# Kernel optimization log

Measured on AMD Instinct MI355X. Metric: run time of the kernel, lower is better.

The kernel has to match this reference:

```python
import jax, jax.numpy as jnp
import numpy as np

B, S, D, H = 2, 2048, 1024, 16
EPS = 1e-7  # keras backend epsilon

def setup_inputs() -> dict:
    key = jax.random.key(0)
    ks = jax.random.split(key, 5)
    x = jax.random.normal(ks[0], (B, S, D), dtype=jnp.float32)
    # mem_mask convention: attend where mem_mask == 0 (causal here)
    i = jnp.arange(S)
    causal = (i[None, :] > i[:, None]).astype(jnp.float32)  # 1 = masked
    mem_mask = jnp.broadcast_to(causal[None, None], (B, 1, S, S))
    Wqkv = jax.random.normal(ks[1], (D, 3 * D), dtype=jnp.float32) * (D ** -0.5)
    W_out = jax.random.normal(ks[2], (D, D), dtype=jnp.float32) * (D ** -0.5)
    b_out = jnp.zeros((D,), dtype=jnp.float32)
    scale = jnp.ones((D,), dtype=jnp.float32)
    gate = jax.random.normal(ks[3], (D,), dtype=jnp.float32) * 0.02
    return {"x": x, "mem_mask": mem_mask, "Wqkv": Wqkv, "W_out": W_out,
            "b_out": b_out, "scale": scale, "gate": gate}

def reference(x, mem_mask, Wqkv, W_out, b_out, scale, gate):
    b, s, d = x.shape
    dh = d // H
    h = jnp.einsum('bsd,de->bse', x, Wqkv)
    q, k, v = jnp.split(h, 3, axis=-1)
    def split_heads(t):
        return t.reshape(b, s, H, dh).transpose(0, 2, 1, 3)  # [B,H,S,dh]
    q, k, v = split_heads(q), split_heads(k), split_heads(v)
    q = q * (dh ** -0.5)
    logits = jnp.einsum('bhqd,bhkd->bhqk', q, k)
    logits = logits * (mem_mask == 0.0).astype(logits.dtype)
    weights = jax.nn.relu(logits)
    o = jnp.einsum('bhqk,bhkd->bhqd', weights, v)
    o = o.transpose(0, 2, 1, 3).reshape(b, s, d)  # combine heads
    # Gated RMSNorm
    ms = jnp.mean(o * o, axis=-1, keepdims=True)
    o = scale * o * jax.lax.rsqrt(ms + EPS) * jax.nn.sigmoid(gate * o)
    return jnp.einsum('bsd,de->bse', o, W_out) + b_out
```

## Files before the change

kernel.cpp:

```cpp
#include <hip/hip_runtime.h>
#include <hip/hip_bf16.h>

typedef unsigned short u16;
typedef __attribute__((ext_vector_type(8))) short bf16x8;
typedef __attribute__((ext_vector_type(4))) short short4v;
typedef __attribute__((ext_vector_type(4))) float floatx4;
typedef __attribute__((ext_vector_type(2))) unsigned uint2v;

__device__ __forceinline__ float bf2f(u16 u) {
    unsigned v = ((unsigned)u) << 16;
    return __builtin_bit_cast(float, v);
}
__device__ __forceinline__ u16 f2bf(float f) {
    unsigned u = __builtin_bit_cast(unsigned, f);
    u += 0x7fffu + ((u >> 16) & 1u);
    return (u16)(u >> 16);
}

#define GLDS16(g, l)                                                             \
    __builtin_amdgcn_global_load_lds(                                            \
        (const __attribute__((address_space(1))) void*)(g),                      \
        (__attribute__((address_space(3))) void*)(l), 16, 0, 0)

__global__ __launch_bounds__(256) void prep(const float* __restrict__ x, u16* __restrict__ xb,
                                            const float* __restrict__ Wqkv, u16* __restrict__ WqkvT,
                                            const float* __restrict__ Wout, u16* __restrict__ WoutT) {
    __shared__ u16 t[32][33];
    int blk = blockIdx.x;
    if (blk < 4096) {
        const int i = blk * 256 + threadIdx.x;
        const floatx4 v = ((const floatx4*)x)[i];
        short4v o;
#pragma unroll
        for (int j = 0; j < 4; ++j) o[j] = (short)f2bf(v[j]);
        ((short4v*)xb)[i] = o;
        return;
    }
    const float* in; u16* out; int R, C, bx, by;
    if (blk < 4096 + 3072) { blk -= 4096; in = Wqkv; out = WqkvT; R = 1024; C = 3072; bx = blk % 96; by = blk / 96; }
    else                   { blk -= 7168; in = Wout; out = WoutT; R = 1024; C = 1024; bx = blk & 31; by = blk >> 5; }
    const int c0 = bx * 32, r0 = by * 32;
    const int xx = threadIdx.x & 31, yy = threadIdx.x >> 5;
#pragma unroll
    for (int i = 0; i < 32; i += 8) t[yy + i][xx] = f2bf(in[(size_t)(r0 + yy + i) * C + c0 + xx]);
    __syncthreads();
#pragma unroll
    for (int i = 0; i < 32; i += 8) out[(size_t)(c0 + yy + i) * R + r0 + xx] = t[xx][yy + i];
}

template <int TM, bool BIAS, typename OUT, bool VT>
__global__ __launch_bounds__(256) void gemm_bt(const u16* __restrict__ A, const u16* __restrict__ Bt,
                                               OUT* __restrict__ C, const float* __restrict__ bias,
                                               u16* __restrict__ vtp, int M, int N, int K) {
    constexpr int MI = TM / 32;
    __shared__ u16 sA[TM * 32];
    __shared__ u16 sB[128 * 32];
    const int tid = threadIdx.x;
    const int lane = tid & 63, wave = tid >> 6;
    const int l15 = lane & 15, quad = lane >> 4;
    const int row0 = blockIdx.y * TM, col0 = blockIdx.x * 128;
    const int wm = (wave & 1) * (TM / 2), wn = (wave >> 1) * 64;
    const int c_ = (tid & 3) << 3;
    floatx4 acc[MI][4] = {};
    for (int k0 = 0; k0 < K; k0 += 32) {
#pragma unroll
        for (int it = 0; it < 2; ++it) {
            const int idx = it * 256 + tid;
            const int r = idx >> 2;
            GLDS16(Bt + (size_t)(col0 + r) * K + k0 + c_, sB + idx * 8);
        }
#pragma unroll
        for (int it = 0; it < TM / 64; ++it) {
            const int idx = it * 256 + tid;
            const int r = idx >> 2;
            GLDS16(A + (size_t)(row0 + r) * K + k0 + c_, sA + idx * 8);
        }
        __syncthreads();
        bf16x8 af[MI], bfr[4];
#pragma unroll
        for (int i = 0; i < MI; ++i) af[i] = *(const bf16x8*)(sA + (wm + i * 16 + l15) * 32 + quad * 8);
#pragma unroll
        for (int j = 0; j < 4; ++j) bfr[j] = *(const bf16x8*)(sB + (wn + j * 16 + l15) * 32 + quad * 8);
#pragma unroll
        for (int i = 0; i < MI; ++i)
#pragma unroll
            for (int j = 0; j < 4; ++j)
                acc[i][j] = __builtin_amdgcn_mfma_f32_16x16x32_bf16(af[i], bfr[j], acc[i][j], 0, 0, 0);
        __syncthreads();
    }
#pragma unroll
    for (int i = 0; i < MI; ++i) {
#pragma unroll
        for (int j = 0; j < 4; ++j) {
            const int col = col0 + wn + j * 16 + l15;
            const int row = row0 + wm + i * 16 + quad * 4;
            const float b = BIAS ? bias[col] : 0.f;
            short4v pk;
#pragma unroll
            for (int r = 0; r < 4; ++r) {
                const float v = acc[i][j][r] + b;
                if constexpr (sizeof(OUT) == 2)
                    C[(size_t)(row + r) * N + col] = (OUT)f2bf(v);
                else
                    C[(size_t)(row + r) * N + col] = (OUT)v;
                if constexpr (VT) pk[r] = (short)f2bf(v * 0.125f);
            }
            if constexpr (VT) {
                if (col0 >= 2048) {
                    const int bb = row >> 11, s = row & 2047;
                    const int hd = (col - 2048) >> 6, dh = col & 63;
                    *(short4v*)(vtp + ((size_t)(bb * 16 + hd) * 64 + dh) * 2048 + s) = pk;
                }
            }
        }
    }
}

__device__ __forceinline__ void pack_store(floatx4 s, u16* dst, bool diag, int kgb, int qg) {
    float v0 = fmaxf(s[0], 0.f), v1 = fmaxf(s[1], 0.f);
    float v2 = fmaxf(s[2], 0.f), v3 = fmaxf(s[3], 0.f);
    if (diag) {
        if (kgb + 0 > qg) v0 = 0.f;
        if (kgb + 1 > qg) v1 = 0.f;
        if (kgb + 2 > qg) v2 = 0.f;
        if (kgb + 3 > qg) v3 = 0.f;
    }
    uint2v p;
    p.x = ((__builtin_bit_cast(unsigned, v0) + 0x8000u) >> 16) |
          ((__builtin_bit_cast(unsigned, v1) + 0x8000u) & 0xffff0000u);
    p.y = ((__builtin_bit_cast(unsigned, v2) + 0x8000u) >> 16) |
          ((__builtin_bit_cast(unsigned, v3) + 0x8000u) & 0xffff0000u);
    *(uint2v*)dst = p;
}

__global__ __launch_bounds__(256) void relu_attn(const u16* __restrict__ h, const u16* __restrict__ vt,
                                                 float* __restrict__ o) {
    __shared__ u16 sK[2][64 * 64];
    __shared__ u16 sV[2][64 * 64];
    __shared__ u16 sP[128 * 72];
    const int bid = blockIdx.x;
    const int pr = bid >> 5;
    const int bh = bid & 31;
    const int b = bh >> 4, hd = bh & 15;
    const int qtl = pr, qth = 31 - pr;
    const int tid = threadIdx.x, lane = tid & 63, wave = tid >> 6;
    const int l15 = lane & 15, quad = lane >> 4;
    const int swz = l15 & 7;

    bf16x8 qfl[2], qfh[2];
    {
        const u16* ql = h + (size_t)(b * 2048 + qtl * 64 + wave * 16 + l15) * 3072 + hd * 64;
        const u16* qh = h + (size_t)(b * 2048 + qth * 64 + wave * 16 + l15) * 3072 + hd * 64;
#pragma unroll
        for (int ks = 0; ks < 2; ++ks) {
            qfl[ks] = *(const bf16x8*)(ql + ks * 32 + quad * 8);
            qfh[ks] = *(const bf16x8*)(qh + ks * 32 + quad * 8);
        }
    }

    floatx4 accl[4] = {}, acch[4] = {};
    const u16* kbase = h + (size_t)(b * 2048) * 3072 + 1024 + hd * 64;
    const u16* vbase = vt + (size_t)bh * 64 * 2048;
    const int qg = wave * 16 + l15;

    auto stage = [&](int kc, int bufi) {
#pragma unroll
        for (int it = 0; it < 2; ++it) {
            const int idx = it * 256 + tid;
            const int r = idx >> 3;
            const int cg = (idx & 7) ^ (r & 7);
            GLDS16(kbase + (size_t)(kc * 64 + r) * 3072 + cg * 8, &sK[bufi][idx * 8]);
            GLDS16(vbase + (size_t)r * 2048 + kc * 64 + cg * 8, &sV[bufi][idx * 8]);
        }
    };

    stage(0, 0);
    __syncthreads();

    for (int kc = 0; kc <= qth; ++kc) {
        const int cur = kc & 1;
        if (kc < qth) stage(kc + 1, cur ^ 1);
        const u16* sKb = sK[cur];
        const u16* sVb = sV[cur];
        const bool lact = (kc <= qtl);
        const floatx4 z = {0.f, 0.f, 0.f, 0.f};
        const int c0 = kc * 64;
#pragma unroll
        for (int mt = 0; mt < 4; ++mt) {
            const int R = mt * 16 + l15;
            const int cq = quad ^ swz;
            const bf16x8 kf0 = *(const bf16x8*)(sKb + R * 64 + cq * 8);
            const bf16x8 kf1 = *(const bf16x8*)(sKb + R * 64 + (cq ^ 4) * 8);
            const int kgb = mt * 16 + quad * 4;
            floatx4 s = __builtin_amdgcn_mfma_f32_16x16x32_bf16(kf0, qfh[0], z, 0, 0, 0);
            s = __builtin_amdgcn_mfma_f32_16x16x32_bf16(kf1, qfh[1], s, 0, 0, 0);
            pack_store(s, sP + (size_t)(64 + qg) * 72 + kgb, kc == qth, kgb, qg);
            if (lact) {
                floatx4 t = __builtin_amdgcn_mfma_f32_16x16x32_bf16(kf0, qfl[0], z, 0, 0, 0);
                t = __builtin_amdgcn_mfma_f32_16x16x32_bf16(kf1, qfl[1], t, 0, 0, 0);
                pack_store(t, sP + (size_t)qg * 72 + kgb, kc == qtl, kgb, qg);
            }
        }
#pragma unroll
        for (int kb = 0; kb < 2; ++kb) {
            const bf16x8 pfh = *(const bf16x8*)(sP + (size_t)(64 + wave * 16 + l15) * 72 + kb * 32 + quad * 8);
#pragma unroll
            for (int nt = 0; nt < 4; ++nt) {
                const int cv = ((kb << 2) | quad) ^ swz;
                const bf16x8 vf = *(const bf16x8*)(sVb + (nt * 16 + l15) * 64 + cv * 8);
                acch[nt] = __builtin_amdgcn_mfma_f32_16x16x32_bf16(pfh, vf, acch[nt], 0, 0, 0);
                if (lact) {
                    const bf16x8 pfl = *(const bf16x8*)(sP + (size_t)(wave * 16 + l15) * 72 + kb * 32 + quad * 8);
                    accl[nt] = __builtin_amdgcn_mfma_f32_16x16x32_bf16(pfl, vf, accl[nt], 0, 0, 0);
                }
            }
        }
        __syncthreads();
    }
#pragma unroll
    for (int nt = 0; nt < 4; ++nt) {
        const int col = hd * 64 + nt * 16 + l15;
        const int rl = qtl * 64 + wave * 16 + quad * 4;
        const int rh = qth * 64 + wave * 16 + quad * 4;
#pragma unroll
        for (int r = 0; r < 4; ++r) {
            o[(size_t)(b * 2048 + rl + r) * 1024 + col] = accl[nt][r];
            o[(size_t)(b * 2048 + rh + r) * 1024 + col] = acch[nt][r];
        }
    }
}

__global__ __launch_bounds__(256) void rms_gate(const float* __restrict__ o, const float* __restrict__ scale,
                                                const float* __restrict__ gate, u16* __restrict__ out) {
    const int row = blockIdx.x;
    const int tid = threadIdx.x;
    const floatx4* op = (const floatx4*)(o + (size_t)row * 1024);
    floatx4 v = op[tid];
    float ss = v[0] * v[0] + v[1] * v[1] + v[2] * v[2] + v[3] * v[3];
#pragma unroll
    for (int m = 32; m >= 1; m >>= 1) ss += __shfl_xor(ss, m, 64);
    __shared__ float red[4];
    if ((tid & 63) == 0) red[tid >> 6] = ss;
    __syncthreads();
    const float ms = (red[0] + red[1] + red[2] + red[3]) * (1.0f / 1024.0f);
    const float inv = rsqrtf(ms + 1e-7f);
    const int c = tid * 4;
#pragma unroll
    for (int j = 0; j < 4; ++j) {
        const float s = scale[c + j];
        const float g = gate[c + j];
        const float x = v[j];
        const float sig = 1.0f / (1.0f + __expf(-g * x));
        out[(size_t)row * 1024 + c + j] = f2bf(s * x * inv * sig);
    }
}

extern "C" void kernel_launch(void* const* d_in, const int* in_sizes, int n_in,
                              void* d_out, int out_size, void* d_ws, size_t ws_size,
                              hipStream_t stream) {
    const float* x     = (const float*)d_in[0];
    const float* Wqkv  = (const float*)d_in[2];
    const float* Wout  = (const float*)d_in[3];
    const float* bout  = (const float*)d_in[4];
    const float* scale = (const float*)d_in[5];
    const float* gate  = (const float*)d_in[6];
    float* out = (float*)d_out;

    char* p = (char*)d_ws;
    u16* xb    = (u16*)p; p += (size_t)4096 * 1024 * 2;
    u16* h     = (u16*)p; p += (size_t)4096 * 3072 * 2;
    u16* vt    = (u16*)p; p += (size_t)32 * 64 * 2048 * 2;
    u16* WqkvT = (u16*)p; p += (size_t)3072 * 1024 * 2;
    u16* WoutT = (u16*)p; p += (size_t)1024 * 1024 * 2;
    float* oat = (float*)p; p += (size_t)4096 * 1024 * 4;
    u16* onorm = (u16*)p; p += (size_t)4096 * 1024 * 2;

    prep<<<8192, 256, 0, stream>>>(x, xb, Wqkv, WqkvT, Wout, WoutT);
    gemm_bt<128, false, u16, true><<<dim3(24, 32), 256, 0, stream>>>(xb, WqkvT, h, nullptr, vt, 4096, 3072, 1024);
    relu_attn<<<512, 256, 0, stream>>>(h, vt, oat);
    rms_gate<<<4096, 256, 0, stream>>>(oat, scale, gate, onorm);
    gemm_bt<64, true, float, false><<<dim3(8, 64), 256, 0, stream>>>(onorm, WoutT, out, bout, nullptr, 4096, 1024, 1024);
}
```

Baseline: 216.5 us.

## Triple-buffer K/V staging in relu_attn with explicit vmcnt waits and one barrier

```diff
diff --git a/kernel.cpp b/kernel.cpp
--- a/kernel.cpp
+++ b/kernel.cpp
@@ -135,8 +135,8 @@
 
 __global__ __launch_bounds__(256) void relu_attn(const u16* __restrict__ h, const u16* __restrict__ vt,
                                                  float* __restrict__ o) {
-    __shared__ u16 sK[2][64 * 64];
-    __shared__ u16 sV[2][64 * 64];
+    __shared__ u16 sK[3][64 * 64];
+    __shared__ u16 sV[3][64 * 64];
     __shared__ u16 sP[128 * 72];
     const int bid = blockIdx.x;
     const int pr = bid >> 5;
@@ -163,28 +163,43 @@
     const u16* vbase = vt + (size_t)bh * 64 * 2048;
     const int qg = wave * 16 + l15;
 
-    auto stage = [&](int kc, int bufi) {
+    const u16* kq[2]; const u16* vq[2]; int lo[2];
+#pragma unroll
+    for (int it = 0; it < 2; ++it) {
+        const int idx = it * 256 + tid;
+        const int r = idx >> 3;
+        const int cg = (idx & 7) ^ (r & 7);
+        kq[it] = kbase + (size_t)r * 3072 + cg * 8;
+        vq[it] = vbase + (size_t)r * 2048 + cg * 8;
+        lo[it] = idx * 8;
+    }
+    auto stage = [&](int bufi) {
 #pragma unroll
         for (int it = 0; it < 2; ++it) {
-            const int idx = it * 256 + tid;
-            const int r = idx >> 3;
-            const int cg = (idx & 7) ^ (r & 7);
-            GLDS16(kbase + (size_t)(kc * 64 + r) * 3072 + cg * 8, &sK[bufi][idx * 8]);
-            GLDS16(vbase + (size_t)r * 2048 + kc * 64 + cg * 8, &sV[bufi][idx * 8]);
+            GLDS16(kq[it], &sK[bufi][lo[it]]);
+            GLDS16(vq[it], &sV[bufi][lo[it]]);
+            kq[it] += 64 * 3072;
+            vq[it] += 64;
         }
     };
 
-    stage(0, 0);
-    __syncthreads();
+    stage(0);
+    stage(1);
+    int bc = 0, bn = 1, bs = 2;
 
     for (int kc = 0; kc <= qth; ++kc) {
-        const int cur = kc & 1;
-        if (kc < qth) stage(kc + 1, cur ^ 1);
-        const u16* sKb = sK[cur];
-        const u16* sVb = sV[cur];
+        if (kc < qth) asm volatile("s_waitcnt vmcnt(4)" ::: "memory");
+        else          asm volatile("s_waitcnt vmcnt(0)" ::: "memory");
+        __builtin_amdgcn_s_barrier();
+        asm volatile("" ::: "memory");
+        __builtin_amdgcn_sched_barrier(0);
+        if (kc + 2 <= qth) stage(bs);
+
+        const u16* sKb = sK[bc];
+        const u16* sVb = sV[bc];
         const bool lact = (kc <= qtl);
         const floatx4 z = {0.f, 0.f, 0.f, 0.f};
-        const int c0 = kc * 64;
+        __builtin_amdgcn_s_setprio(1);
 #pragma unroll
         for (int mt = 0; mt < 4; ++mt) {
             const int R = mt * 16 + l15;
@@ -215,7 +230,8 @@
                 }
             }
         }
-        __syncthreads();
+        __builtin_amdgcn_s_setprio(0);
+        int t_ = bc; bc = bn; bn = bs; bs = t_;
     }
 #pragma unroll
     for (int nt = 0; nt < 4; ++nt) {
```

Result: no change. 219.7 us (+1.5%).
